# Performance work log

Hardware: AMD Instinct MI355X
Metric: run time of the kernel (lower is better)

## Reference

```python
import jax, jax.numpy as jnp
import numpy as np

N, E, G = 10000, 160000, 64          # nodes, edges, graphs
T, FIN, ED, FOUT = 5, 75, 50, 15     # towers, channels, edge-emb dim, per-tower out
EPS_BN, EPS_STD = 1e-5, 1e-5


def setup_inputs() -> dict:
    key = jax.random.key(0)
    ks = jax.random.split(key, 16)
    s = 0.05
    return dict(
        x=jax.random.randint(ks[0], (N,), 0, 21),
        edge_index=jax.random.randint(ks[1], (2, E), 0, N),
        edge_attr=jax.random.randint(ks[2], (E,), 0, 4),
        batch=jnp.sort(jax.random.randint(ks[3], (N,), 0, G)),
        node_emb=jax.random.normal(ks[4], (21, FIN), dtype=jnp.float32),
        edge_emb=jax.random.normal(ks[5], (4, ED), dtype=jnp.float32),
        We=jax.random.normal(ks[6], (4, ED, FIN), dtype=jnp.float32) * s,
        be=jnp.zeros((4, FIN), jnp.float32),
        Wpre=jax.random.normal(ks[7], (4, T, 3 * FIN, FIN), dtype=jnp.float32) * s,
        bpre=jnp.zeros((4, T, FIN), jnp.float32),
        Wpost=jax.random.normal(ks[8], (4, T, 13 * FIN, FOUT), dtype=jnp.float32) * s,
        bpost=jnp.zeros((4, T, FOUT), jnp.float32),
        Wlin=jax.random.normal(ks[9], (4, FIN, FIN), dtype=jnp.float32) * s,
        blin=jnp.zeros((4, FIN), jnp.float32),
        bn_gamma=jnp.ones((4, FIN), jnp.float32),
        bn_beta=jnp.zeros((4, FIN), jnp.float32),
        uaf=jnp.array([1.1, -0.01, 1e-5, -0.9, 1e-5], dtype=jnp.float32),
        mW1=jax.random.normal(ks[10], (FIN, 50), dtype=jnp.float32) * s,
        mb1=jnp.zeros((50,), jnp.float32),
        mW2=jax.random.normal(ks[11], (50, 25), dtype=jnp.float32) * s,
        mb2=jnp.zeros((25,), jnp.float32),
        mW3=jax.random.normal(ks[12], (25, 1), dtype=jnp.float32) * s,
        mb3=jnp.zeros((1,), jnp.float32),
    )


def _uaf(v, p):
    # softplus(A*(x+B) + C*x^2) - softplus(D*(x-B)) + E
    return (jax.nn.softplus(p[0] * (v + p[1]) + p[2] * v * v)
            - jax.nn.softplus(p[3] * (v - p[1])) + p[4])


def _pna_layer(h, src, dst, e_feat, We, be, Wpre, bpre, Wpost, bpost, Wl, bl,
               deg, avg_log):
    eemb = e_feat @ We + be                      # [E, FIN] edge encoder
    x_i, x_j = h[dst], h[src]                    # [E, FIN] gathers
    # pre-MLP: per-tower Linear(cat[x_i, x_j, e], 3F -> F), split weight blocks
    W1, W2, W3 = Wpre[:, :FIN], Wpre[:, FIN:2 * FIN], Wpre[:, 2 * FIN:]
    m = (jnp.einsum('ec,tcf->etf', x_i, W1)
         + jnp.einsum('ec,tcf->etf', x_j, W2)
         + jnp.einsum('ec,tcf->etf', eemb, W3) + bpre)   # [E, T, FIN]
    degc = jnp.maximum(deg, 1.0)[:, None, None]
    mean = jax.ops.segment_sum(m, dst, N) / degc          # [N, T, FIN]
    mean_sq = jax.ops.segment_sum(m * m, dst, N) / degc
    empty = (deg == 0.0)[:, None, None]
    mn = jnp.where(empty, 0.0, jax.ops.segment_min(m, dst, N))
    mx = jnp.where(empty, 0.0, jax.ops.segment_max(m, dst, N))
    std = jnp.sqrt(jax.nn.relu(mean_sq - mean * mean) + EPS_STD)
    agg = jnp.concatenate([mean, mn, mx, std], axis=-1)   # [N, T, 4F]
    amp = (jnp.log(jnp.maximum(deg, 1.0) + 1.0) / avg_log)[:, None, None]
    out = jnp.concatenate([agg, agg * amp, agg / amp], axis=-1)  # [N, T, 12F]
    # cat tower input (divide_input=False -> full x per tower)
    out = jnp.concatenate(
        [jnp.broadcast_to(h[:, None, :], (N, T, FIN)), out], axis=-1)  # [N,T,13F]
    out = jnp.einsum('ntc,tcf->ntf', out, Wpost) + bpost  # [N, T, FOUT]
    return out.reshape(N, T * FOUT) @ Wl + bl             # [N, FIN]


def reference(node_emb, edge_emb, We, be, Wpre, bpre, Wpost, bpost, Wlin, blin,
              bn_gamma, bn_beta, uaf, mW1, mb1, mW2, mb2, mW3, mb3,
              x, edge_index, edge_attr, batch):
    src, dst = edge_index[0], edge_index[1]
    h = node_emb[x]                              # [N, 75]
    e_feat = edge_emb[edge_attr]                 # [E, 50]
    deg = jax.ops.segment_sum(jnp.ones((E,), h.dtype), dst, N)
    avg_log = jnp.mean(jnp.log(deg + 1.0))       # PNA avg degree (log) statistic
    for l in range(4):
        out = _pna_layer(h, src, dst, e_feat, We[l], be[l], Wpre[l], bpre[l],
                         Wpost[l], bpost[l], Wlin[l], blin[l], deg, avg_log)
        mu = out.mean(axis=0)
        var = out.var(axis=0)                    # biased, training-mode BN
        out = (out - mu) * jax.lax.rsqrt(var + EPS_BN) * bn_gamma[l] + bn_beta[l]
        h = _uaf(out, uaf)
    pooled = jax.ops.segment_sum(h, batch, G)    # global_add_pool -> [G, 75]
    z = _uaf(pooled @ mW1 + mb1, uaf)
    z = _uaf(z @ mW2 + mb2, uaf)
    return z @ mW3 + mb3                         # [G, 1]
```

## Files before the change

### kernel.cpp

```cpp
#include <hip/hip_runtime.h>
#include <hip/hip_fp16.h>
#include <math.h>

static constexpr int N_   = 10000;
static constexpr int E_   = 160000;
static constexpr int G_   = 64;
static constexpr int T_   = 5;
static constexpr int FIN_ = 75;
static constexpr int ED_  = 50;
static constexpr int FOUT_= 15;
static constexpr int TF_  = T_*FIN_;
static constexpr int AGGW_= 4*FIN_;
static constexpr int YC_  = 48;
static constexpr int NP_  = 10112;
static constexpr int AW_  = 400;
static constexpr int BW_  = 384;
static constexpr int WK_  = 380;

__device__ __forceinline__ float softplus_f(float x){
    return fmaxf(x, 0.f) + log1pf(expf(-fabsf(x)));
}
__device__ __forceinline__ float uaf_f(float v, const float* __restrict__ p){
    return softplus_f(p[0]*(v + p[1]) + p[2]*v*v) - softplus_f(p[3]*(v - p[1])) + p[4];
}
__device__ __forceinline__ unsigned pack2h(float a, float b){
    __half2 h = __floats2half2_rn(a, b);
    return *reinterpret_cast<unsigned*>(&h);
}

__global__ void k_h0(const int* __restrict__ x, const float* __restrict__ node_emb, float* __restrict__ hT){
    int i = blockIdx.x*blockDim.x + threadIdx.x;
    if (i >= 80*N_) return;
    int q = i / N_, n = i % N_;
    hT[(size_t)q*NP_ + n] = (q < FIN_) ? node_emb[x[n]*FIN_ + q] : 0.f;
}

__global__ void k_deg(const int* __restrict__ ei, int* __restrict__ deg_i){
    int e = blockIdx.x*blockDim.x + threadIdx.x;
    if (e >= E_) return;
    atomicAdd(&deg_i[ei[E_ + e]], 1);
}

__global__ void k_scan(const int* __restrict__ deg_i, int* __restrict__ offs, float* __restrict__ avglog){
    __shared__ int sd[1024];
    __shared__ float sf[1024];
    __shared__ int carry;
    if (threadIdx.x == 0) carry = 0;
    __syncthreads();
    float ls = 0.f;
    for (int base = 0; base < N_; base += 1024){
        int i = base + threadIdx.x;
        int v = (i < N_) ? deg_i[i] : 0;
        if (i < N_) ls += logf((float)v + 1.f);
        sd[threadIdx.x] = v;
        __syncthreads();
        for (int off = 1; off < 1024; off <<= 1){
            int t = (threadIdx.x >= off) ? sd[threadIdx.x - off] : 0;
            __syncthreads();
            sd[threadIdx.x] += t;
            __syncthreads();
        }
        if (i < N_) offs[i] = carry + sd[threadIdx.x] - v;
        __syncthreads();
        if (threadIdx.x == 0) carry += sd[1023];
        __syncthreads();
    }
    if (threadIdx.x == 0) offs[N_] = carry;
    sf[threadIdx.x] = ls;
    __syncthreads();
    for (int off = 512; off > 0; off >>= 1){
        if (threadIdx.x < off) sf[threadIdx.x] += sf[threadIdx.x + off];
        __syncthreads();
    }
    if (threadIdx.x == 0) avglog[0] = sf[0] / (float)N_;
}

__global__ void k_fill(const int* __restrict__ ei, const int* __restrict__ eattr,
                       const int* __restrict__ offs, int* __restrict__ cursor, int* __restrict__ csr){
    int e = blockIdx.x*blockDim.x + threadIdx.x;
    if (e >= E_) return;
    int d = ei[E_ + e];
    int pos = offs[d] + atomicAdd(&cursor[d], 1);
    csr[pos] = ei[e] | (eattr[e] << 16);
}

__global__ void k_amp(const int* __restrict__ deg_i, const float* __restrict__ avglog,
                      float* __restrict__ ampv, float* __restrict__ iampv){
    int n = blockIdx.x*blockDim.x + threadIdx.x;
    if (n >= N_) return;
    float dm = fmaxf((float)deg_i[n], 1.f);
    float a = logf(dm + 1.f) / avglog[0];
    ampv[n] = a;
    iampv[n] = 1.f / a;
}

__global__ void k_eemb(const float* __restrict__ edge_emb, const float* __restrict__ We,
                       const float* __restrict__ be, float* __restrict__ eembw){
    int i = blockIdx.x*blockDim.x + threadIdx.x;
    if (i >= 4*4*FIN_) return;
    int c = i % FIN_;
    int a = (i / FIN_) % 4;
    int l = i / (4*FIN_);
    float s = be[l*FIN_ + c];
    for (int k = 0; k < ED_; k++) s = fmaf(edge_emb[a*ED_ + k], We[(l*ED_ + k)*FIN_ + c], s);
    eembw[i] = s;
}

__global__ void k_tbl(const float* __restrict__ eembw, const float* __restrict__ Wpre,
                      const float* __restrict__ bpre, float* __restrict__ tbl){
    int i = blockIdx.x*blockDim.x + threadIdx.x;
    if (i >= 4*4*TF_) return;
    int f = i % FIN_;
    int t = (i / FIN_) % T_;
    int a = (i / TF_) % 4;
    int l = i / (4*TF_);
    float s = bpre[(l*T_ + t)*FIN_ + f];
    const float* em = eembw + (l*4 + a)*FIN_;
    const float* W3 = Wpre + ((size_t)(l*T_ + t)*225 + 2*FIN_)*FIN_;
    for (int c = 0; c < FIN_; c++) s = fmaf(em[c], W3[c*FIN_ + f], s);
    tbl[i] = s;
}

__global__ void k_wcomb(const float* __restrict__ Wpost, float* __restrict__ Wcomb){
    int i = blockIdx.x*blockDim.x + threadIdx.x;
    if (i >= 4*T_*WK_*YC_) return;
    int j = i % YC_;
    int c = (i / YC_) % WK_;
    int t = (i / (YC_*WK_)) % T_;
    int l = i / (YC_*WK_*T_);
    float v = 0.f;
    if (j < 45){
        int blk = j / 15, fo = j % 15;
        const float* Wp = Wpost + (size_t)(l*T_ + t)*975*15;
        if (c < FIN_){ if (blk == 0) v = Wp[c*15 + fo]; }
        else if (c >= 80){
            int r = c - 80;
            int fi = r >> 2, kind = r & 3;
            v = Wp[(FIN_ + blk*AGGW_ + kind*FIN_ + fi)*15 + fo];
        }
    }
    Wcomb[i] = v;
}

__global__ void k_wpre80(const float* __restrict__ Wpre, float* __restrict__ Wpre80){
    int i = blockIdx.x*blockDim.x + threadIdx.x;
    if (i >= 4*10*80*80) return;
    int c = i % 80;
    int r = (i / 80) % 80;
    int chunk = (i / 6400) % 10;
    int l = i / 64000;
    int t = chunk >> 1, half = chunk & 1;
    float v = 0.f;
    if (r < FIN_ && c < FIN_)
        v = Wpre[((size_t)(l*T_ + t)*225 + half*FIN_ + r)*FIN_ + c];
    Wpre80[i] = v;
}

__global__ void k_wlin80(const float* __restrict__ Wlin, float* __restrict__ Wlin80){
    int i = blockIdx.x*blockDim.x + threadIdx.x;
    if (i >= 4*FIN_*80) return;
    int q = i % 80;
    int p = (i / 80) % FIN_;
    int l = i / (80*FIN_);
    Wlin80[i] = (q < FIN_) ? Wlin[(l*FIN_ + p)*FIN_ + q] : 0.f;
}

__global__ void __launch_bounds__(128) k_A4(const float* __restrict__ hT, const float* __restrict__ Wpre80_l,
                                            float* __restrict__ Af, __half* __restrict__ Bh){
    __shared__ float smem[5760];
    float* ActB = smem;
    float* WtB  = smem + 2560;
    int chunkid = blockIdx.y;
    int t = chunkid >> 1, half = chunkid & 1;
    const float* __restrict__ Wl = Wpre80_l + (size_t)chunkid*6400;
    int n0 = blockIdx.x * 64;
    int tid = threadIdx.x;
    int tn = tid & 15, tj = tid >> 4;

    for (int i = tid; i < 320; i += 128){
        int r = i >> 4, c4 = i & 15;
        *(float4*)(&ActB[r*64 + c4*4]) = *(const float4*)(hT + (size_t)r*NP_ + n0 + c4*4);
    }
    for (int i = tid; i < 400; i += 128){
        int r = i / 20, c4 = i % 20;
        *(float4*)(&WtB[r*80 + c4*4]) = *(const float4*)(Wl + r*80 + c4*4);
    }
    __syncthreads();

    float acc[4][10];
    #pragma unroll
    for (int m = 0; m < 4; m++)
        #pragma unroll
        for (int j = 0; j < 10; j++) acc[m][j] = 0.f;

    float4 ph0, ph1, ph2, pw0, pw1, pw2, pw3;
    #pragma unroll 1
    for (int ch = 0; ch < 4; ch++){
        int buf = ch & 1;
        bool have = (ch + 1 < 4);
        if (have){
            const float* sp = hT + (size_t)((ch+1)*20)*NP_ + n0;
            { int i0 = tid;       ph0 = *(const float4*)(sp + (size_t)(i0 >> 4)*NP_ + (i0 & 15)*4); }
            { int i1 = tid + 128; ph1 = *(const float4*)(sp + (size_t)(i1 >> 4)*NP_ + (i1 & 15)*4); }
            if (tid < 64){ int i2 = tid + 256; ph2 = *(const float4*)(sp + (size_t)(i2 >> 4)*NP_ + (i2 & 15)*4); }
            const float* wp = Wl + (ch+1)*1600;
            { int i = tid;       pw0 = *(const float4*)(wp + (i/20)*80 + (i%20)*4); }
            { int i = tid + 128; pw1 = *(const float4*)(wp + (i/20)*80 + (i%20)*4); }
            { int i = tid + 256; pw2 = *(const float4*)(wp + (i/20)*80 + (i%20)*4); }
            if (tid < 16){ int i = tid + 384; pw3 = *(const float4*)(wp + (i/20)*80 + (i%20)*4); }
        }
        const float* A  = ActB + buf*1280;
        const float* Wb = WtB + buf*1600;
        #pragma unroll
        for (int k = 0; k < 20; k++){
            float4 av = *(const float4*)(A + (k<<6) + (tn<<2));
            const float2* wr = (const float2*)(Wb + k*80 + tj*10);
            float wv[10];
            #pragma unroll
            for (int j2 = 0; j2 < 5; j2++){ float2 w2 = wr[j2]; wv[2*j2] = w2.x; wv[2*j2+1] = w2.y; }
            #pragma unroll
            for (int j = 0; j < 10; j++){
                acc[0][j] = fmaf(av.x, wv[j], acc[0][j]);
                acc[1][j] = fmaf(av.y, wv[j], acc[1][j]);
                acc[2][j] = fmaf(av.z, wv[j], acc[2][j]);
                acc[3][j] = fmaf(av.w, wv[j], acc[3][j]);
            }
        }
        if (have){
            float* Ad = ActB + (buf ^ 1)*1280;
            float* Wd = WtB + (buf ^ 1)*1600;
            { int i0 = tid;       *(float4*)(&Ad[(i0 >> 4)*64 + (i0 & 15)*4]) = ph0; }
            { int i1 = tid + 128; *(float4*)(&Ad[(i1 >> 4)*64 + (i1 & 15)*4]) = ph1; }
            if (tid < 64){ int i2 = tid + 256; *(float4*)(&Ad[(i2 >> 4)*64 + (i2 & 15)*4]) = ph2; }
            { int i = tid;       *(float4*)(&Wd[(i/20)*80 + (i%20)*4]) = pw0; }
            { int i = tid + 128; *(float4*)(&Wd[(i/20)*80 + (i%20)*4]) = pw1; }
            { int i = tid + 256; *(float4*)(&Wd[(i/20)*80 + (i%20)*4]) = pw2; }
            if (tid < 16){ int i = tid + 384; *(float4*)(&Wd[(i/20)*80 + (i%20)*4]) = pw3; }
            __syncthreads();
        }
    }
    __syncthreads();
    float* Out = smem;
    #pragma unroll
    for (int m = 0; m < 4; m++)
        #pragma unroll
        for (int j = 0; j < 10; j++)
            Out[(tn*4 + m)*81 + tj*10 + j] = acc[m][j];
    __syncthreads();
    if (half == 0){
        for (int i = tid; i < 64*20; i += 128){
            int node = i / 20, q4 = i % 20;
            int gn = n0 + node;
            if (gn < N_){
                const float* src = Out + node*81 + q4*4;
                *(float4*)(Af + (size_t)gn*AW_ + t*80 + q4*4) = make_float4(src[0], src[1], src[2], src[3]);
            }
        }
    } else {
        for (int i = tid; i < 64*38; i += 128){
            int node = i / 38, q = i % 38;
            int gn = n0 + node;
            if (gn < N_){
                const float* src = Out + node*81 + 2*q;
                *(unsigned*)((__half*)Bh + (size_t)gn*BW_ + t*76 + 2*q) = pack2h(src[0], src[1]);
            }
        }
    }
}

__global__ void __launch_bounds__(128) k_agg(const float* __restrict__ Af, const __half* __restrict__ Bh,
                                             const int* __restrict__ offs, const int* __restrict__ csr,
                                             const float* __restrict__ tbl_l, uint2* __restrict__ agg2h){
    __shared__ float tl[4*TF_];
    int bid = blockIdx.x;
    int n = (bid & 7)*1250 + (bid >> 3);
    for (int idx = threadIdx.x; idx < 4*TF_; idx += 128) tl[idx] = tbl_l[idx];
    __syncthreads();
    int s = offs[n], e_end = offs[n+1];
    int f0 = threadIdx.x;
    int f1 = threadIdx.x + 128;
    int f2r = threadIdx.x + 256;
    int f2 = (f2r < TF_) ? f2r : 0;
    int aoA0 = (f0/FIN_)*80 + f0%FIN_;
    int aoA1 = (f1/FIN_)*80 + f1%FIN_;
    int aoA2 = (f2/FIN_)*80 + f2%FIN_;
    int aoB0 = (f0/FIN_)*76 + f0%FIN_;
    int aoB1 = (f1/FIN_)*76 + f1%FIN_;
    int aoB2 = (f2/FIN_)*76 + f2%FIN_;
    const float* An = Af + (size_t)n*AW_;
    float a0 = An[aoA0], a1 = An[aoA1], a2 = An[aoA2];
    float s0=0.f,s1=0.f,s2=0.f, q0=0.f,q1=0.f,q2=0.f;
    float mn0=INFINITY,mn1=INFINITY,mn2=INFINITY;
    float mx0=-INFINITY,mx1=-INFINITY,mx2=-INFINITY;
    int e = s;
    for (; e + 3 < e_end; e += 4){
        float b0[4], b1[4], b2[4];
        const float* tt[4];
        #pragma unroll
        for (int u = 0; u < 4; u++){
            int pk = csr[e + u];
            const __half* B = Bh + (size_t)(pk & 0xFFFF)*BW_;
            tt[u] = tl + (pk >> 16)*TF_;
            b0[u] = __half2float(B[aoB0]);
            b1[u] = __half2float(B[aoB1]);
            b2[u] = __half2float(B[aoB2]);
        }
        #pragma unroll
        for (int u = 0; u < 4; u++){
            float m0 = a0 + b0[u] + tt[u][f0];
            float m1 = a1 + b1[u] + tt[u][f1];
            float m2 = a2 + b2[u] + tt[u][f2];
            s0 += m0; s1 += m1; s2 += m2;
            q0 = fmaf(m0,m0,q0); q1 = fmaf(m1,m1,q1); q2 = fmaf(m2,m2,q2);
            mn0 = fminf(mn0,m0); mx0 = fmaxf(mx0,m0);
            mn1 = fminf(mn1,m1); mx1 = fmaxf(mx1,m1);
            mn2 = fminf(mn2,m2); mx2 = fmaxf(mx2,m2);
        }
    }
    for (; e < e_end; e++){
        int pk = csr[e];
        const __half* B = Bh + (size_t)(pk & 0xFFFF)*BW_;
        const float* t0 = tl + (pk >> 16)*TF_;
        float m0 = a0 + __half2float(B[aoB0]) + t0[f0];
        float m1 = a1 + __half2float(B[aoB1]) + t0[f1];
        float m2 = a2 + __half2float(B[aoB2]) + t0[f2];
        s0 += m0; q0 = fmaf(m0,m0,q0); mn0 = fminf(mn0,m0); mx0 = fmaxf(mx0,m0);
        s1 += m1; q1 = fmaf(m1,m1,q1); mn1 = fminf(mn1,m1); mx1 = fmaxf(mx1,m1);
        s2 += m2; q2 = fmaf(m2,m2,q2); mn2 = fminf(mn2,m2); mx2 = fmaxf(mx2,m2);
    }
    float deg = (float)(e_end - s);
    float dc = fmaxf(deg, 1.f);
    float inv = 1.f / dc;
    bool empty = (deg == 0.f);
    {
        float mean = s0*inv;
        float sd = sqrtf(fmaxf(q0*inv - mean*mean, 0.f) + 1e-5f);
        int t = f0/FIN_, fi = f0%FIN_;
        uint2 o; o.x = pack2h(mean, empty?0.f:mn0); o.y = pack2h(empty?0.f:mx0, sd);
        agg2h[(size_t)(t*FIN_+fi)*NP_ + n] = o;
    }
    {
        float mean = s1*inv;
        float sd = sqrtf(fmaxf(q1*inv - mean*mean, 0.f) + 1e-5f);
        int t = f1/FIN_, fi = f1%FIN_;
        uint2 o; o.x = pack2h(mean, empty?0.f:mn1); o.y = pack2h(empty?0.f:mx1, sd);
        agg2h[(size_t)(t*FIN_+fi)*NP_ + n] = o;
    }
    if (f2r < TF_){
        float mean = s2*inv;
        float sd = sqrtf(fmaxf(q2*inv - mean*mean, 0.f) + 1e-5f);
        int t = f2r/FIN_, fi = f2r%FIN_;
        uint2 o; o.x = pack2h(mean, empty?0.f:mn2); o.y = pack2h(empty?0.f:mx2, sd);
        agg2h[(size_t)(t*FIN_+fi)*NP_ + n] = o;
    }
}

__device__ __forceinline__ void unp4_64(float* Ad, int i, uint2 u){
    int fq = i >> 6, n = i & 63;
    __half2 lo = *reinterpret_cast<__half2*>(&u.x);
    __half2 hi = *reinterpret_cast<__half2*>(&u.y);
    Ad[(fq*4+0)*64 + n] = __low2float(lo);
    Ad[(fq*4+1)*64 + n] = __high2float(lo);
    Ad[(fq*4+2)*64 + n] = __low2float(hi);
    Ad[(fq*4+3)*64 + n] = __high2float(hi);
}

__global__ void __launch_bounds__(128) k_post6(const float* __restrict__ hT, const uint2* __restrict__ agg2h,
                                               const float* __restrict__ Wcomb_l,
                                               float* __restrict__ Yp0, float* __restrict__ Yp1){
    __shared__ float Act[2][20*64];
    __shared__ float Wt[2][20*YC_];
    int t = blockIdx.y;
    int kz = blockIdx.z;
    int c0 = kz ? 9 : 0;
    int c1 = kz ? 19 : 9;
    float* __restrict__ Yp = kz ? Yp1 : Yp0;
    int n0 = blockIdx.x * 64;
    int tid = threadIdx.x;
    int tn = tid & 15, tj = tid >> 4;
    const float* __restrict__ Wl = Wcomb_l + (size_t)t*WK_*YC_;
    const uint2* __restrict__ agt = agg2h + (size_t)t*FIN_*NP_;

    if (c0 < 4){
        const float* sp = hT + (size_t)(c0*20)*NP_ + n0;
        for (int i = tid; i < 320; i += 128){
            int r = i >> 4, c4 = i & 15;
            *(float4*)(&Act[0][r*64 + c4*4]) = *(const float4*)(sp + (size_t)r*NP_ + c4*4);
        }
    } else {
        const uint2* sp = agt + (size_t)((c0 - 4)*5)*NP_ + n0;
        for (int i = tid; i < 320; i += 128)
            unp4_64(Act[0], i, sp[(size_t)(i >> 6)*NP_ + (i & 63)]);
    }
    for (int i = tid; i < 240; i += 128){
        int r = i / 12, c4 = i % 12;
        *(float4*)(&Wt[0][r*YC_ + c4*4]) = *(const float4*)(Wl + (size_t)(c0*20 + r)*YC_ + c4*4);
    }
    __syncthreads();

    float acc[4][6];
    #pragma unroll
    for (int m = 0; m < 4; m++)
        #pragma unroll
        for (int j = 0; j < 6; j++) acc[m][j] = 0.f;

    float4 ph0, ph1, ph2, pw0, pw1;
    uint2  pb0, pb1, pb2;
    #pragma unroll 1
    for (int ch = c0; ch < c1; ch++){
        int buf = (ch - c0) & 1;
        int ch1 = ch + 1;
        bool have = (ch1 < c1);
        bool nh = (ch1 < 4);
        if (have){
            if (nh){
                const float* sp = hT + (size_t)(ch1*20)*NP_ + n0;
                { int i0 = tid;       ph0 = *(const float4*)(sp + (size_t)(i0 >> 4)*NP_ + (i0 & 15)*4); }
                { int i1 = tid + 128; ph1 = *(const float4*)(sp + (size_t)(i1 >> 4)*NP_ + (i1 & 15)*4); }
                if (tid < 64){ int i2 = tid + 256; ph2 = *(const float4*)(sp + (size_t)(i2 >> 4)*NP_ + (i2 & 15)*4); }
            } else {
                const uint2* sp = agt + (size_t)((ch1 - 4)*5)*NP_ + n0;
                { int i0 = tid;       pb0 = sp[(size_t)(i0 >> 6)*NP_ + (i0 & 63)]; }
                { int i1 = tid + 128; pb1 = sp[(size_t)(i1 >> 6)*NP_ + (i1 & 63)]; }
                if (tid < 64){ int i2 = tid + 256; pb2 = sp[(size_t)(i2 >> 6)*NP_ + (i2 & 63)]; }
            }
            { int i = tid; int r = i / 12, c4 = i % 12;
              pw0 = *(const float4*)(Wl + (size_t)(ch1*20 + r)*YC_ + c4*4); }
            if (tid < 112){ int i = tid + 128; int r = i / 12, c4 = i % 12;
              pw1 = *(const float4*)(Wl + (size_t)(ch1*20 + r)*YC_ + c4*4); }
        }
        const float* A = Act[buf];
        const float* Wb = Wt[buf];
        #pragma unroll
        for (int k = 0; k < 20; k++){
            float4 av = *(const float4*)(A + (k<<6) + (tn<<2));
            const float* wr = Wb + k*YC_ + tj*6;
            #pragma unroll
            for (int j = 0; j < 6; j++){
                float wv = wr[j];
                acc[0][j] = fmaf(av.x, wv, acc[0][j]);
                acc[1][j] = fmaf(av.y, wv, acc[1][j]);
                acc[2][j] = fmaf(av.z, wv, acc[2][j]);
                acc[3][j] = fmaf(av.w, wv, acc[3][j]);
            }
        }
        if (have){
            float* Ad = Act[buf ^ 1];
            float* Wd = Wt[buf ^ 1];
            if (nh){
                { int i0 = tid;       *(float4*)(&Ad[(i0 >> 4)*64 + (i0 & 15)*4]) = ph0; }
                { int i1 = tid + 128; *(float4*)(&Ad[(i1 >> 4)*64 + (i1 & 15)*4]) = ph1; }
                if (tid < 64){ int i2 = tid + 256; *(float4*)(&Ad[(i2 >> 4)*64 + (i2 & 15)*4]) = ph2; }
            } else {
                unp4_64(Ad, tid, pb0);
                unp4_64(Ad, tid + 128, pb1);
                if (tid < 64) unp4_64(Ad, tid + 256, pb2);
            }
            { int i = tid; int r = i / 12, c4 = i % 12; *(float4*)(&Wd[r*YC_ + c4*4]) = pw0; }
            if (tid < 112){ int i = tid + 128; int r = i / 12, c4 = i % 12; *(float4*)(&Wd[r*YC_ + c4*4]) = pw1; }
            __syncthreads();
        }
    }
    int nodeb = n0 + tn*4;
    #pragma unroll
    for (int j = 0; j < 6; j++){
        int col = t*YC_ + tj*6 + j;
        float4 v = make_float4(acc[0][j], acc[1][j], acc[2][j], acc[3][j]);
        if (nodeb + 3 < N_){
            *(float4*)(Yp + (size_t)col*NP_ + nodeb) = v;
        } else {
            #pragma unroll
            for (int m = 0; m < 4; m++)
                if (nodeb + m < N_) Yp[(size_t)col*NP_ + nodeb + m] = (&v.x)[m];
        }
    }
}

__global__ void __launch_bounds__(64) k_Y(const float* __restrict__ Yp0, const float* __restrict__ Yp1,
                                          const float* __restrict__ ampv,
                                          const float* __restrict__ iampv, const float* __restrict__ bpost_l,
                                          const float* __restrict__ Wlin80_l, const float* __restrict__ blin_l,
                                          float* __restrict__ olinT, float* __restrict__ bnsum, float* __restrict__ bnsq){
    __shared__ float st[64*77];
    int qbase = blockIdx.y * 40;
    int qcnt  = blockIdx.y ? 35 : 40;
    int n = blockIdx.x*64 + threadIdx.x;
    int nn = (n < N_) ? n : N_-1;
    bool valid = (n < N_);
    float amp = ampv[nn], iamp = iampv[nn];
    #pragma unroll 1
    for (int t = 0; t < T_; t++){
        #pragma unroll
        for (int fo = 0; fo < FOUT_; fo++){
            size_t b0 = (size_t)(t*YC_ + fo)*NP_ + nn;
            size_t b1 = (size_t)(t*YC_ + 15 + fo)*NP_ + nn;
            size_t b2 = (size_t)(t*YC_ + 30 + fo)*NP_ + nn;
            float v = (Yp0[b0] + Yp1[b0])
                    + amp  * (Yp0[b1] + Yp1[b1])
                    + iamp * (Yp0[b2] + Yp1[b2])
                    + bpost_l[t*FOUT_ + fo];
            st[threadIdx.x*77 + t*FOUT_ + fo] = v;
        }
    }
    __syncthreads();
    float acc[40];
    #pragma unroll
    for (int k = 0; k < 40; k++) acc[k] = (qbase + k < FIN_) ? blin_l[qbase + k] : 0.f;
    #pragma unroll 1
    for (int p = 0; p < FIN_; p++){
        float yv = st[threadIdx.x*77 + p];
        const float* Wp = Wlin80_l + p*80 + qbase;
        #pragma unroll
        for (int k = 0; k < 40; k++) acc[k] = fmaf(yv, Wp[k], acc[k]);
    }
    if (valid){
        #pragma unroll
        for (int k = 0; k < 40; k++){
            int q = qbase + k;
            if (q < FIN_) olinT[(size_t)q*NP_ + n] = acc[k];
        }
    }
    __syncthreads();
    #pragma unroll
    for (int k = 0; k < 40; k++) st[threadIdx.x*77 + k] = valid ? acc[k] : 0.f;
    __syncthreads();
    for (int qq = threadIdx.x; qq < qcnt; qq += 64){
        float s = 0.f, s2 = 0.f;
        #pragma unroll 4
        for (int m = 0; m < 64; m++){ float v = st[m*77 + qq]; s += v; s2 = fmaf(v, v, s2); }
        atomicAdd(&bnsum[qbase + qq], s);
        atomicAdd(&bnsq[qbase + qq], s2);
    }
}

__global__ void k_bn(const float* __restrict__ olinT, const float* __restrict__ bnsum, const float* __restrict__ bnsq,
                     const float* __restrict__ gamma_l, const float* __restrict__ beta_l,
                     const float* __restrict__ uafp, float* __restrict__ hT){
    int i = blockIdx.x*blockDim.x + threadIdx.x;
    if (i >= FIN_*N_) return;
    int q = i / N_, n = i % N_;
    float mu = bnsum[q] * (1.f/(float)N_);
    float var = bnsq[q] * (1.f/(float)N_) - mu*mu;
    float xh = (olinT[(size_t)q*NP_ + n] - mu) * rsqrtf(var + 1e-5f) * gamma_l[q] + beta_l[q];
    hT[(size_t)q*NP_ + n] = uaf_f(xh, uafp);
}

__global__ void __launch_bounds__(256) k_pool2(const float* __restrict__ hT, const int* __restrict__ batch,
                                               float* __restrict__ pooled){
    __shared__ int sb[2];
    int g = blockIdx.x;
    if (threadIdx.x < 2){
        int key = g + threadIdx.x;
        int lo = 0, hi = N_;
        while (lo < hi){ int mid = (lo + hi) >> 1; if (batch[mid] < key) lo = mid + 1; else hi = mid; }
        sb[threadIdx.x] = lo;
    }
    __syncthreads();
    int s = sb[0], e = sb[1];
    int wave = threadIdx.x >> 6, lane = threadIdx.x & 63;
    for (int q = wave; q < FIN_; q += 4){
        float sum = 0.f;
        for (int n = s + lane; n < e; n += 64) sum += hT[(size_t)q*NP_ + n];
        #pragma unroll
        for (int off = 32; off > 0; off >>= 1) sum += __shfl_down(sum, off);
        if (lane == 0) pooled[g*FIN_ + q] = sum;
    }
}

__global__ void __launch_bounds__(64) k_mlp(const float* __restrict__ pooled,
        const float* __restrict__ mW1, const float* __restrict__ mb1,
        const float* __restrict__ mW2, const float* __restrict__ mb2,
        const float* __restrict__ mW3, const float* __restrict__ mb3,
        const float* __restrict__ uafp, float* __restrict__ outp){
    __shared__ float pr[FIN_];
    __shared__ float z1[50];
    __shared__ float z2[25];
    int g = blockIdx.x;
    for (int c = threadIdx.x; c < FIN_; c += 64) pr[c] = pooled[g*FIN_ + c];
    __syncthreads();
    if (threadIdx.x < 50){
        float s = mb1[threadIdx.x];
        for (int c = 0; c < FIN_; c++) s = fmaf(pr[c], mW1[c*50 + threadIdx.x], s);
        z1[threadIdx.x] = uaf_f(s, uafp);
    }
    __syncthreads();
    if (threadIdx.x < 25){
        float s = mb2[threadIdx.x];
        for (int c = 0; c < 50; c++) s = fmaf(z1[c], mW2[c*25 + threadIdx.x], s);
        z2[threadIdx.x] = uaf_f(s, uafp);
    }
    __syncthreads();
    if (threadIdx.x == 0){
        float s = mb3[0];
        for (int c = 0; c < 25; c++) s = fmaf(z2[c], mW3[c], s);
        outp[g] = s;
    }
}

extern "C" void kernel_launch(void* const* d_in, const int* in_sizes, int n_in,
                              void* d_out, int out_size, void* d_ws, size_t ws_size,
                              hipStream_t stream) {
    const int* x         = (const int*)d_in[0];
    const int* ei        = (const int*)d_in[1];
    const int* eattr     = (const int*)d_in[2];
    const int* batch     = (const int*)d_in[3];
    const float* node_emb= (const float*)d_in[4];
    const float* edge_emb= (const float*)d_in[5];
    const float* We      = (const float*)d_in[6];
    const float* be      = (const float*)d_in[7];
    const float* Wpre    = (const float*)d_in[8];
    const float* bpre    = (const float*)d_in[9];
    const float* Wpost   = (const float*)d_in[10];
    const float* bpost   = (const float*)d_in[11];
    const float* Wlin    = (const float*)d_in[12];
    const float* blin    = (const float*)d_in[13];
    const float* bn_gamma= (const float*)d_in[14];
    const float* bn_beta = (const float*)d_in[15];
    const float* uafp    = (const float*)d_in[16];
    const float* mW1     = (const float*)d_in[17];
    const float* mb1     = (const float*)d_in[18];
    const float* mW2     = (const float*)d_in[19];
    const float* mb2     = (const float*)d_in[20];
    const float* mW3     = (const float*)d_in[21];
    const float* mb3     = (const float*)d_in[22];
    float* outp          = (float*)d_out;

    char* w = (char*)d_ws;
    auto alloc = [&](size_t bytes) -> void* {
        void* p = (void*)w;
        w += (bytes + 255) & ~(size_t)255;
        return p;
    };
    float*  hT    = (float*)alloc((size_t)80*NP_*4);
    float*  Af    = (float*)alloc((size_t)N_*AW_*4);
    __half* Bh    = (__half*)alloc((size_t)N_*BW_*2);
    uint2*  agg2h = (uint2*)alloc((size_t)TF_*NP_*8);
    float*  Yp0   = (float*)alloc((size_t)T_*YC_*NP_*4);
    float*  Yp1   = (float*)alloc((size_t)T_*YC_*NP_*4);
    float*  olinT = (float*)alloc((size_t)FIN_*NP_*4);
    float*  ampv  = (float*)alloc(N_*4);
    float*  iampv = (float*)alloc(N_*4);
    float*  avglog= (float*)alloc(4);
    float*  tbl   = (float*)alloc(4*4*TF_*4);
    float*  eembw = (float*)alloc(4*4*FIN_*4);
    float*  Wcomb = (float*)alloc((size_t)4*T_*WK_*YC_*4);
    float*  Wpre80= (float*)alloc((size_t)4*10*80*80*4);
    float*  Wlin80= (float*)alloc(4*FIN_*80*4);
    float*  bnsum = (float*)alloc(2*FIN_*4);
    float*  bnsq  = bnsum + FIN_;
    float*  pooled= (float*)alloc(G_*FIN_*4);
    int* deg_i   = (int*)alloc(N_*4);
    int* offs    = (int*)alloc((N_+1)*4);
    int* cursor  = (int*)alloc(N_*4);
    int* csr     = (int*)alloc(E_*4);

    hipMemsetAsync(deg_i, 0, N_*4, stream);
    hipMemsetAsync(cursor, 0, N_*4, stream);

    k_h0<<<(80*N_ + 255)/256, 256, 0, stream>>>(x, node_emb, hT);
    k_deg<<<(E_ + 255)/256, 256, 0, stream>>>(ei, deg_i);
    k_scan<<<1, 1024, 0, stream>>>(deg_i, offs, avglog);
    k_fill<<<(E_ + 255)/256, 256, 0, stream>>>(ei, eattr, offs, cursor, csr);
    k_amp<<<(N_ + 255)/256, 256, 0, stream>>>(deg_i, avglog, ampv, iampv);
    k_eemb<<<(4*4*FIN_ + 255)/256, 256, 0, stream>>>(edge_emb, We, be, eembw);
    k_tbl<<<(4*4*TF_ + 255)/256, 256, 0, stream>>>(eembw, Wpre, bpre, tbl);
    k_wcomb<<<(4*T_*WK_*YC_ + 255)/256, 256, 0, stream>>>(Wpost, Wcomb);
    k_wpre80<<<(4*10*80*80 + 255)/256, 256, 0, stream>>>(Wpre, Wpre80);
    k_wlin80<<<(4*FIN_*80 + 255)/256, 256, 0, stream>>>(Wlin, Wlin80);

    int nab = NP_/64;
    int npb = (N_ + 63)/64;
    for (int l = 0; l < 4; l++){
        hipMemsetAsync(bnsum, 0, 2*FIN_*4, stream);
        k_A4<<<dim3(nab, 10), 128, 0, stream>>>(hT, Wpre80 + (size_t)l*10*6400, Af, Bh);
        k_agg<<<N_, 128, 0, stream>>>(Af, Bh, offs, csr, tbl + (size_t)l*4*TF_, agg2h);
        k_post6<<<dim3(npb, T_, 2), 128, 0, stream>>>(hT, agg2h, Wcomb + (size_t)l*T_*WK_*YC_, Yp0, Yp1);
        k_Y<<<dim3(npb, 2), 64, 0, stream>>>(Yp0, Yp1, ampv, iampv, bpost + l*T_*FOUT_,
                                             Wlin80 + (size_t)l*FIN_*80, blin + l*FIN_,
                                             olinT, bnsum, bnsq);
        k_bn<<<(FIN_*N_ + 255)/256, 256, 0, stream>>>(olinT, bnsum, bnsq,
                                                      bn_gamma + l*FIN_, bn_beta + l*FIN_, uafp, hT);
    }

    k_pool2<<<G_, 256, 0, stream>>>(hT, batch, pooled);
    k_mlp<<<G_, 64, 0, stream>>>(pooled, mW1, mb1, mW2, mb2, mW3, mb3, uafp, outp);
}
```

Before: 875.9 us.

## Stage full Wpre chunk in LDS and stream activations via global_load_lds

The pre-MLP GEMM kernel now loads its whole 80x80 weight chunk into shared memory once at the start, instead of double-buffering it in 20-row slices. Activation tiles for the next k-chunk are copied straight from global memory into LDS with the async global_load_lds builtin, split across the two waves. This removes the register staging and the explicit LDS stores in the main loop, aiming to overlap the copies with the FMA work. The cost is more shared memory per block (about 36 KB instead of 23 KB), which can lower occupancy, plus a barrier on every loop iteration.

```diff
diff --git a/kernel.cpp b/kernel.cpp
--- a/kernel.cpp
+++ b/kernel.cpp
@@ -165,26 +165,25 @@
     Wlin80[i] = (q < FIN_) ? Wlin[(l*FIN_ + p)*FIN_ + q] : 0.f;
 }
 
-__global__ void __launch_bounds__(128) k_A4(const float* __restrict__ hT, const float* __restrict__ Wpre80_l,
+__global__ void __launch_bounds__(128) k_A5(const float* __restrict__ hT, const float* __restrict__ Wpre80_l,
                                             float* __restrict__ Af, __half* __restrict__ Bh){
-    __shared__ float smem[5760];
-    float* ActB = smem;
-    float* WtB  = smem + 2560;
+    __shared__ float smem[8960];
+    float* Wt   = smem;
+    float* ActB = smem + 6400;
     int chunkid = blockIdx.y;
     int t = chunkid >> 1, half = chunkid & 1;
     const float* __restrict__ Wl = Wpre80_l + (size_t)chunkid*6400;
     int n0 = blockIdx.x * 64;
     int tid = threadIdx.x;
     int tn = tid & 15, tj = tid >> 4;
-
+    int wv = tid >> 6, ln = tid & 63;
+
+    for (int i = tid; i < 1600; i += 128)
+        *(float4*)(&Wt[i*4]) = *(const float4*)(Wl + i*4);
     for (int i = tid; i < 320; i += 128){
         int r = i >> 4, c4 = i & 15;
         *(float4*)(&ActB[r*64 + c4*4]) = *(const float4*)(hT + (size_t)r*NP_ + n0 + c4*4);
     }
-    for (int i = tid; i < 400; i += 128){
-        int r = i / 20, c4 = i % 20;
-        *(float4*)(&WtB[r*80 + c4*4]) = *(const float4*)(Wl + r*80 + c4*4);
-    }
     __syncthreads();
 
     float acc[4][10];
@@ -193,53 +192,49 @@
         #pragma unroll
         for (int j = 0; j < 10; j++) acc[m][j] = 0.f;
 
-    float4 ph0, ph1, ph2, pw0, pw1, pw2, pw3;
     #pragma unroll 1
     for (int ch = 0; ch < 4; ch++){
         int buf = ch & 1;
-        bool have = (ch + 1 < 4);
-        if (have){
-            const float* sp = hT + (size_t)((ch+1)*20)*NP_ + n0;
-            { int i0 = tid;       ph0 = *(const float4*)(sp + (size_t)(i0 >> 4)*NP_ + (i0 & 15)*4); }
-            { int i1 = tid + 128; ph1 = *(const float4*)(sp + (size_t)(i1 >> 4)*NP_ + (i1 & 15)*4); }
-            if (tid < 64){ int i2 = tid + 256; ph2 = *(const float4*)(sp + (size_t)(i2 >> 4)*NP_ + (i2 & 15)*4); }
-            const float* wp = Wl + (ch+1)*1600;
-            { int i = tid;       pw0 = *(const float4*)(wp + (i/20)*80 + (i%20)*4); }
-            { int i = tid + 128; pw1 = *(const float4*)(wp + (i/20)*80 + (i%20)*4); }
-            { int i = tid + 256; pw2 = *(const float4*)(wp + (i/20)*80 + (i%20)*4); }
-            if (tid < 16){ int i = tid + 384; pw3 = *(const float4*)(wp + (i/20)*80 + (i%20)*4); }
-        }
-        const float* A  = ActB + buf*1280;
-        const float* Wb = WtB + buf*1600;
+        if (ch < 3){
+            const float* srcb = hT + (size_t)((ch+1)*20)*NP_ + n0;
+            float* dstb = ActB + (buf ^ 1)*1280;
+            int r0 = (ln >> 4), c = (ln & 15)*4;
+            if (wv == 0){
+                #pragma unroll
+                for (int s = 0; s < 3; s++)
+                    __builtin_amdgcn_global_load_lds(
+                        (const __attribute__((address_space(1))) unsigned*)(srcb + (size_t)(s*4 + r0)*NP_ + c),
+                        (__attribute__((address_space(3))) unsigned*)(dstb + s*256),
+                        16, 0, 0);
+            } else {
+                #pragma unroll
+                for (int s = 3; s < 5; s++)
+                    __builtin_amdgcn_global_load_lds(
+                        (const __attribute__((address_space(1))) unsigned*)(srcb + (size_t)(s*4 + r0)*NP_ + c),
+                        (__attribute__((address_space(3))) unsigned*)(dstb + s*256),
+                        16, 0, 0);
+            }
+        }
+        const float* A = ActB + buf*1280;
+        const float* Wc = Wt + ch*20*80;
         #pragma unroll
         for (int k = 0; k < 20; k++){
             float4 av = *(const float4*)(A + (k<<6) + (tn<<2));
-            const float2* wr = (const float2*)(Wb + k*80 + tj*10);
-            float wv[10];
+            const float2* wr = (const float2*)(Wc + k*80 + tj*10);
+            float wvv[10];
             #pragma unroll
-            for (int j2 = 0; j2 < 5; j2++){ float2 w2 = wr[j2]; wv[2*j2] = w2.x; wv[2*j2+1] = w2.y; }
+            for (int j2 = 0; j2 < 5; j2++){ float2 w2 = wr[j2]; wvv[2*j2] = w2.x; wvv[2*j2+1] = w2.y; }
             #pragma unroll
             for (int j = 0; j < 10; j++){
-                acc[0][j] = fmaf(av.x, wv[j], acc[0][j]);
-                acc[1][j] = fmaf(av.y, wv[j], acc[1][j]);
-                acc[2][j] = fmaf(av.z, wv[j], acc[2][j]);
-                acc[3][j] = fmaf(av.w, wv[j], acc[3][j]);
+                acc[0][j] = fmaf(av.x, wvv[j], acc[0][j]);
+                acc[1][j] = fmaf(av.y, wvv[j], acc[1][j]);
+                acc[2][j] = fmaf(av.z, wvv[j], acc[2][j]);
+                acc[3][j] = fmaf(av.w, wvv[j], acc[3][j]);
             }
         }
-        if (have){
-            float* Ad = ActB + (buf ^ 1)*1280;
-            float* Wd = WtB + (buf ^ 1)*1600;
-            { int i0 = tid;       *(float4*)(&Ad[(i0 >> 4)*64 + (i0 & 15)*4]) = ph0; }
-            { int i1 = tid + 128; *(float4*)(&Ad[(i1 >> 4)*64 + (i1 & 15)*4]) = ph1; }
-            if (tid < 64){ int i2 = tid + 256; *(float4*)(&Ad[(i2 >> 4)*64 + (i2 & 15)*4]) = ph2; }
-            { int i = tid;       *(float4*)(&Wd[(i/20)*80 + (i%20)*4]) = pw0; }
-            { int i = tid + 128; *(float4*)(&Wd[(i/20)*80 + (i%20)*4]) = pw1; }
-            { int i = tid + 256; *(float4*)(&Wd[(i/20)*80 + (i%20)*4]) = pw2; }
-            if (tid < 16){ int i = tid + 384; *(float4*)(&Wd[(i/20)*80 + (i%20)*4]) = pw3; }
-            __syncthreads();
-        }
-    }
-    __syncthreads();
+        __syncthreads();
+    }
+
     float* Out = smem;
     #pragma unroll
     for (int m = 0; m < 4; m++)
@@ -672,7 +667,7 @@
     int npb = (N_ + 63)/64;
     for (int l = 0; l < 4; l++){
         hipMemsetAsync(bnsum, 0, 2*FIN_*4, stream);
-        k_A4<<<dim3(nab, 10), 128, 0, stream>>>(hT, Wpre80 + (size_t)l*10*6400, Af, Bh);
+        k_A5<<<dim3(nab, 10), 128, 0, stream>>>(hT, Wpre80 + (size_t)l*10*6400, Af, Bh);
         k_agg<<<N_, 128, 0, stream>>>(Af, Bh, offs, csr, tbl + (size_t)l*4*TF_, agg2h);
         k_post6<<<dim3(npb, T_, 2), 128, 0, stream>>>(hT, agg2h, Wcomb + (size_t)l*T_*WK_*YC_, Yp0, Yp1);
         k_Y<<<dim3(npb, 2), 64, 0, stream>>>(Yp0, Yp1, ampv, iampv, bpost + l*T_*FOUT_,
```

New measurement: 833.9 us. 1.05x faster.
